# Optimization experiments

Measured on AMD Instinct MI355X. Metric: run time of the kernel, lower is better.

## Reference

```python
import jax, jax.numpy as jnp
import numpy as np

N_QUBITS = 4
N_LAYERS = 6
NUM_CLASSES = 10


def _apply_1q(state, gate, wire):
    # state: (B,2,2,2,2); gate: (2,2) shared or (B,2,2) per-sample
    s = jnp.moveaxis(state, wire + 1, -1)
    if gate.ndim == 3:
        s = jnp.einsum('bij,b...j->b...i', gate, s)
    else:
        s = jnp.einsum('ij,b...j->b...i', gate, s)
    return jnp.moveaxis(s, -1, wire + 1)


def _apply_cnot(state, c, t):
    s = jnp.moveaxis(state, (c + 1, t + 1), (-2, -1))
    s = jnp.stack([s[..., 0, :], s[..., 1, ::-1]], axis=-2)
    return jnp.moveaxis(s, (-2, -1), (c + 1, t + 1))


def _rot(phi, theta, omega):
    # PennyLane Rot = RZ(omega) @ RY(theta) @ RZ(phi)
    c, s = jnp.cos(theta / 2), jnp.sin(theta / 2)
    ep = jnp.exp(-0.5j * (phi + omega))
    em = jnp.exp(-0.5j * (phi - omega))
    return jnp.stack([
        jnp.stack([ep * c, -jnp.conj(em) * s]),
        jnp.stack([em * s, jnp.conj(ep) * c]),
    ])


def _quantum_net(angles, q_weights):
    # batched default.qubit statevector simulation, 4 wires
    B = angles.shape[0]
    state = jnp.zeros((B, 2, 2, 2, 2), jnp.complex64).at[:, 0, 0, 0, 0].set(1.0)
    # AngleEmbedding, rotation='Y' (per-sample RY gates)
    for w in range(N_QUBITS):
        a = angles[:, w]
        c, s = jnp.cos(a / 2), jnp.sin(a / 2)
        g = jnp.stack([jnp.stack([c, -s], -1), jnp.stack([s, c], -1)], -2)
        state = _apply_1q(state, g.astype(jnp.complex64), w)
    # StronglyEntanglingLayers: Rot on each wire, then ring of CNOTs with range r
    for l in range(N_LAYERS):
        for w in range(N_QUBITS):
            state = _apply_1q(state, _rot(q_weights[l, w, 0], q_weights[l, w, 1], q_weights[l, w, 2]), w)
        r = l % (N_QUBITS - 1) + 1
        for w in range(N_QUBITS):
            state = _apply_cnot(state, w, (w + r) % N_QUBITS)
    probs = jnp.abs(state) ** 2  # (B,2,2,2,2)
    z = jnp.array([1.0, -1.0], dtype=probs.dtype)
    exps = [jnp.einsum('bijkl,' + 'ijkl'[w] + '->b', probs, z) for w in range(N_QUBITS)]
    return jnp.stack(exps, -1)  # (B,4) expval PauliZ per wire


def setup_inputs() -> dict:
    key = jax.random.key(0)
    ks = jax.random.split(key, 6)
    B = 65536
    x = jax.random.normal(ks[0], (B, 512), jnp.float32)
    W_pre = jax.random.normal(ks[1], (N_QUBITS, 512), jnp.float32) / np.sqrt(512)
    b_pre = jax.random.normal(ks[2], (N_QUBITS,), jnp.float32) * 0.01
    q_weights = 0.01 * jax.random.normal(ks[3], (N_LAYERS, N_QUBITS, 3), jnp.float32)
    W_post = jax.random.normal(ks[4], (NUM_CLASSES, N_QUBITS), jnp.float32) / np.sqrt(N_QUBITS)
    b_post = jax.random.normal(ks[5], (NUM_CLASSES,), jnp.float32) * 0.01
    return {'x': x, 'W_pre': W_pre, 'b_pre': b_pre, 'q_weights': q_weights,
            'W_post': W_post, 'b_post': b_post}


def reference(x, W_pre, b_pre, q_weights, W_post, b_post):
    pre = x @ W_pre.T + b_pre                 # (B,4)
    angles = jnp.tanh(pre) * np.float32(np.pi)
    q_out = _quantum_net(angles, q_weights)   # (B,4)
    return q_out @ W_post.T + b_post          # (B,10)
```

## Files before the change

### kernel.cpp

```cpp
#include <hip/hip_runtime.h>
#include <math.h>

#define BLOCK 256
#define WAVES_PER_BLOCK 4
#define ROWS_PER_WAVE 8
#define ROWS_PER_BLOCK 32
#define K 512
#define K4 128
#define NQ 4
#define NL 6
#define NC 10

__global__ __launch_bounds__(BLOCK, 4) void vqc_fused_kernel(
    const float* __restrict__ x,
    const float* __restrict__ W_pre,
    const float* __restrict__ b_pre,
    const float* __restrict__ q_weights,
    const float* __restrict__ W_post,
    const float* __restrict__ b_post,
    float* __restrict__ out)
{
    __shared__ float gates[NL * NQ][8];
    __shared__ float angles_s[ROWS_PER_BLOCK][NQ];
    __shared__ float Wpost_s[NC * NQ];
    __shared__ float bpost_s[NC];
    __shared__ float bpre_s[NQ];

    const int tid  = threadIdx.x;
    const int wave = tid >> 6;
    const int lane = tid & 63;

    if (tid < NL * NQ) {
        const int l = tid >> 2, w = tid & 3;
        const float phi = q_weights[l * 12 + w * 3 + 0];
        const float th  = q_weights[l * 12 + w * 3 + 1];
        const float om  = q_weights[l * 12 + w * 3 + 2];
        const float c  = cosf(0.5f * th), s = sinf(0.5f * th);
        const float hp = 0.5f * (phi + om), hm = 0.5f * (phi - om);
        const float epr = cosf(hp), epi = -sinf(hp);
        const float emr = cosf(hm), emi = -sinf(hm);
        gates[tid][0] =  epr * c;  gates[tid][1] =  epi * c;
        gates[tid][2] = -emr * s;  gates[tid][3] =  emi * s;
        gates[tid][4] =  emr * s;  gates[tid][5] =  emi * s;
        gates[tid][6] =  epr * c;  gates[tid][7] = -epi * c;
    }
    if (tid >= 64 && tid < 64 + NC * NQ) Wpost_s[tid - 64] = W_post[tid - 64];
    if (tid >= 104 && tid < 104 + NC)    bpost_s[tid - 104] = b_post[tid - 104];
    if (tid >= 114 && tid < 114 + NQ)    bpre_s[tid - 114]  = b_pre[tid - 114];
    __syncthreads();

    const float4* x4 = (const float4*)x;
    const float4* W4 = (const float4*)W_pre;
    const float4 w0a = W4[0 * K4 + lane], w0b = W4[0 * K4 + 64 + lane];
    const float4 w1a = W4[1 * K4 + lane], w1b = W4[1 * K4 + 64 + lane];
    const float4 w2a = W4[2 * K4 + lane], w2b = W4[2 * K4 + 64 + lane];
    const float4 w3a = W4[3 * K4 + lane], w3b = W4[3 * K4 + 64 + lane];

    const int rowBase = blockIdx.x * ROWS_PER_BLOCK + wave * ROWS_PER_WAVE;

    #pragma unroll 4
    for (int rr = 0; rr < ROWS_PER_WAVE; ++rr) {
        const int r = rowBase + rr;
        const float4* xrow = x4 + (size_t)r * K4;
        const float4 xa = xrow[lane];
        const float4 xb = xrow[64 + lane];
        float acc0 = xa.x * w0a.x + xa.y * w0a.y + xa.z * w0a.z + xa.w * w0a.w
                   + xb.x * w0b.x + xb.y * w0b.y + xb.z * w0b.z + xb.w * w0b.w;
        float acc1 = xa.x * w1a.x + xa.y * w1a.y + xa.z * w1a.z + xa.w * w1a.w
                   + xb.x * w1b.x + xb.y * w1b.y + xb.z * w1b.z + xb.w * w1b.w;
        float acc2 = xa.x * w2a.x + xa.y * w2a.y + xa.z * w2a.z + xa.w * w2a.w
                   + xb.x * w2b.x + xb.y * w2b.y + xb.z * w2b.z + xb.w * w2b.w;
        float acc3 = xa.x * w3a.x + xa.y * w3a.y + xa.z * w3a.z + xa.w * w3a.w
                   + xb.x * w3b.x + xb.y * w3b.y + xb.z * w3b.z + xb.w * w3b.w;
        #pragma unroll
        for (int m = 1; m < 64; m <<= 1) {
            acc0 += __shfl_xor(acc0, m);
            acc1 += __shfl_xor(acc1, m);
            acc2 += __shfl_xor(acc2, m);
            acc3 += __shfl_xor(acc3, m);
        }
        if (lane < NQ) {
            const float accj = (lane == 0) ? acc0 : (lane == 1) ? acc1
                             : (lane == 2) ? acc2 : acc3;
            angles_s[wave * ROWS_PER_WAVE + rr][lane] =
                tanhf(accj + bpre_s[lane]) * 3.14159265358979323846f;
        }
    }
    __syncthreads();

    if (tid < ROWS_PER_BLOCK) {
        const int rl = tid;
        const int r  = blockIdx.x * ROWS_PER_BLOCK + rl;
        const float a0 = angles_s[rl][0], a1 = angles_s[rl][1];
        const float a2 = angles_s[rl][2], a3 = angles_s[rl][3];
        float c0, s0, c1, s1, c2, s2, c3, s3;
        __sincosf(0.5f * a0, &s0, &c0);
        __sincosf(0.5f * a1, &s1, &c1);
        __sincosf(0.5f * a2, &s2, &c2);
        __sincosf(0.5f * a3, &s3, &c3);

        float ar[16], ai[16];
        #pragma unroll
        for (int i = 0; i < 16; ++i) {
            ar[i] = ((i & 8) ? s0 : c0) * ((i & 4) ? s1 : c1)
                  * ((i & 2) ? s2 : c2) * ((i & 1) ? s3 : c3);
            ai[i] = 0.f;
        }

        #pragma unroll
        for (int l = 0; l < NL; ++l) {
            #pragma unroll
            for (int w = 0; w < NQ; ++w) {
                const float* G = gates[l * 4 + w];
                const float g00r = G[0], g00i = G[1], g01r = G[2], g01i = G[3];
                const float g10r = G[4], g10i = G[5], g11r = G[6], g11i = G[7];
                const int m = 8 >> w;
                #pragma unroll
                for (int i0 = 0; i0 < 16; ++i0) {
                    if (i0 & m) continue;
                    const int i1 = i0 | m;
                    const float A0r = ar[i0], A0i = ai[i0];
                    const float A1r = ar[i1], A1i = ai[i1];
                    ar[i0] = g00r * A0r - g00i * A0i + g01r * A1r - g01i * A1i;
                    ai[i0] = g00r * A0i + g00i * A0r + g01r * A1i + g01i * A1r;
                    ar[i1] = g10r * A0r - g10i * A0i + g11r * A1r - g11i * A1i;
                    ai[i1] = g10r * A0i + g10i * A0r + g11r * A1i + g11i * A1r;
                }
            }
            const int rshift = l % 3 + 1;
            #pragma unroll
            for (int w = 0; w < NQ; ++w) {
                const int cm = 8 >> w;
                const int tm = 8 >> ((w + rshift) & 3);
                #pragma unroll
                for (int i = 0; i < 16; ++i) {
                    if ((i & cm) && !(i & tm)) {
                        const int ii = i | tm;
                        float t;
                        t = ar[i]; ar[i] = ar[ii]; ar[ii] = t;
                        t = ai[i]; ai[i] = ai[ii]; ai[ii] = t;
                    }
                }
            }
        }

        float e0 = 0.f, e1 = 0.f, e2 = 0.f, e3 = 0.f;
        #pragma unroll
        for (int i = 0; i < 16; ++i) {
            const float p = ar[i] * ar[i] + ai[i] * ai[i];
            e0 += (i & 8) ? -p : p;
            e1 += (i & 4) ? -p : p;
            e2 += (i & 2) ? -p : p;
            e3 += (i & 1) ? -p : p;
        }

        float* orow = out + (size_t)r * NC;
        #pragma unroll
        for (int c = 0; c < NC; ++c) {
            orow[c] = bpost_s[c]
                    + Wpost_s[c * 4 + 0] * e0 + Wpost_s[c * 4 + 1] * e1
                    + Wpost_s[c * 4 + 2] * e2 + Wpost_s[c * 4 + 3] * e3;
        }
    }
}

extern "C" void kernel_launch(void* const* d_in, const int* in_sizes, int n_in,
                              void* d_out, int out_size, void* d_ws, size_t ws_size,
                              hipStream_t stream) {
    const float* x         = (const float*)d_in[0];
    const float* W_pre     = (const float*)d_in[1];
    const float* b_pre     = (const float*)d_in[2];
    const float* q_weights = (const float*)d_in[3];
    const float* W_post    = (const float*)d_in[4];
    const float* b_post    = (const float*)d_in[5];
    float* out = (float*)d_out;

    const int B = in_sizes[0] / K;
    dim3 grid(B / ROWS_PER_BLOCK);
    vqc_fused_kernel<<<grid, BLOCK, 0, stream>>>(x, W_pre, b_pre, q_weights,
                                                 W_post, b_post, out);
}
```

Measured before the change: 214.9 us.

## Split prenet GEMV and quantum simulation into separate kernels with full thread use

Splits the fused kernel in two. The first kernel computes the pre-net projection, prefetching the next row and using a transposed shuffle reduction that needs fewer shuffles, then writes the angles to workspace. The second kernel simulates the quantum circuit with one thread per row, so all 256 threads do work instead of only 32 per block sitting idle behind a barrier. The split adds a second launch and a small round trip through global memory; the first kernel also swaps tanhf for an exp-based approximation and the second writes its output with float2 stores.

```diff
diff --git a/kernel.cpp b/kernel.cpp
--- a/kernel.cpp
+++ b/kernel.cpp
@@ -1,34 +1,98 @@
 #include <hip/hip_runtime.h>
 #include <math.h>
 
-#define BLOCK 256
-#define WAVES_PER_BLOCK 4
-#define ROWS_PER_WAVE 8
-#define ROWS_PER_BLOCK 32
 #define K 512
 #define K4 128
 #define NQ 4
 #define NL 6
 #define NC 10
 
-__global__ __launch_bounds__(BLOCK, 4) void vqc_fused_kernel(
+#define A_BLOCK 256
+#define A_ROWS_PER_WAVE 8
+#define A_ROWS_PER_BLOCK 32
+
+__global__ __launch_bounds__(A_BLOCK, 4) void prenet_kernel(
     const float* __restrict__ x,
     const float* __restrict__ W_pre,
     const float* __restrict__ b_pre,
+    float* __restrict__ angles)
+{
+    const int tid  = threadIdx.x;
+    const int wave = tid >> 6;
+    const int lane = tid & 63;
+
+    const float4* x4 = (const float4*)x;
+    const float4* W4 = (const float4*)W_pre;
+    const float4 w0a = W4[0 * K4 + lane], w0b = W4[0 * K4 + 64 + lane];
+    const float4 w1a = W4[1 * K4 + lane], w1b = W4[1 * K4 + 64 + lane];
+    const float4 w2a = W4[2 * K4 + lane], w2b = W4[2 * K4 + 64 + lane];
+    const float4 w3a = W4[3 * K4 + lane], w3b = W4[3 * K4 + 64 + lane];
+    const float bp = (lane < NQ) ? b_pre[lane] : 0.f;
+
+    const int rowBase = blockIdx.x * A_ROWS_PER_BLOCK + wave * A_ROWS_PER_WAVE;
+    const float4* xrow0 = x4 + (size_t)rowBase * K4;
+    float4 xa = xrow0[lane];
+    float4 xb = xrow0[64 + lane];
+
+    #pragma unroll
+    for (int rr = 0; rr < A_ROWS_PER_WAVE; ++rr) {
+        float4 na = xa, nb = xb;
+        if (rr + 1 < A_ROWS_PER_WAVE) {
+            const float4* nx = x4 + (size_t)(rowBase + rr + 1) * K4;
+            na = nx[lane];
+            nb = nx[64 + lane];
+        }
+
+        float acc0 = xa.x * w0a.x + xa.y * w0a.y + xa.z * w0a.z + xa.w * w0a.w
+                   + xb.x * w0b.x + xb.y * w0b.y + xb.z * w0b.z + xb.w * w0b.w;
+        float acc1 = xa.x * w1a.x + xa.y * w1a.y + xa.z * w1a.z + xa.w * w1a.w
+                   + xb.x * w1b.x + xb.y * w1b.y + xb.z * w1b.z + xb.w * w1b.w;
+        float acc2 = xa.x * w2a.x + xa.y * w2a.y + xa.z * w2a.z + xa.w * w2a.w
+                   + xb.x * w2b.x + xb.y * w2b.y + xb.z * w2b.z + xb.w * w2b.w;
+        float acc3 = xa.x * w3a.x + xa.y * w3a.y + xa.z * w3a.z + xa.w * w3a.w
+                   + xb.x * w3b.x + xb.y * w3b.y + xb.z * w3b.z + xb.w * w3b.w;
+
+        const bool b0 = (lane & 1);
+        float pA = b0 ? acc1 : acc0;
+        float qA = b0 ? acc0 : acc1;
+        pA += __shfl_xor(qA, 1);
+        float pB = b0 ? acc3 : acc2;
+        float qB = b0 ? acc2 : acc3;
+        pB += __shfl_xor(qB, 1);
+        const bool b1 = (lane & 2);
+        float p = b1 ? pB : pA;
+        float q = b1 ? pA : pB;
+        p += __shfl_xor(q, 2);
+        p += __shfl_xor(p, 4);
+        p += __shfl_xor(p, 8);
+        p += __shfl_xor(p, 16);
+        p += __shfl_xor(p, 32);
+
+        if (lane < NQ) {
+            const float z = p + bp;
+            const float e = __expf(2.f * z);
+            const float th = 1.f - 2.f / (e + 1.f);
+            angles[(size_t)(rowBase + rr) * NQ + lane] =
+                th * 3.14159265358979323846f;
+        }
+        xa = na; xb = nb;
+    }
+}
+
+#define B_BLOCK 256
+
+__global__ __launch_bounds__(B_BLOCK, 4) void vqc_kernel(
+    const float* __restrict__ angles,
     const float* __restrict__ q_weights,
     const float* __restrict__ W_post,
     const float* __restrict__ b_post,
     float* __restrict__ out)
 {
     __shared__ float gates[NL * NQ][8];
-    __shared__ float angles_s[ROWS_PER_BLOCK][NQ];
     __shared__ float Wpost_s[NC * NQ];
     __shared__ float bpost_s[NC];
-    __shared__ float bpre_s[NQ];
-
-    const int tid  = threadIdx.x;
-    const int wave = tid >> 6;
-    const int lane = tid & 63;
+
+    const int tid = threadIdx.x;
 
     if (tid < NL * NQ) {
         const int l = tid >> 2, w = tid & 3;
@@ -46,122 +110,83 @@
     }
     if (tid >= 64 && tid < 64 + NC * NQ) Wpost_s[tid - 64] = W_post[tid - 64];
     if (tid >= 104 && tid < 104 + NC)    bpost_s[tid - 104] = b_post[tid - 104];
-    if (tid >= 114 && tid < 114 + NQ)    bpre_s[tid - 114]  = b_pre[tid - 114];
     __syncthreads();
 
-    const float4* x4 = (const float4*)x;
-    const float4* W4 = (const float4*)W_pre;
-    const float4 w0a = W4[0 * K4 + lane], w0b = W4[0 * K4 + 64 + lane];
-    const float4 w1a = W4[1 * K4 + lane], w1b = W4[1 * K4 + 64 + lane];
-    const float4 w2a = W4[2 * K4 + lane], w2b = W4[2 * K4 + 64 + lane];
-    const float4 w3a = W4[3 * K4 + lane], w3b = W4[3 * K4 + 64 + lane];
-
-    const int rowBase = blockIdx.x * ROWS_PER_BLOCK + wave * ROWS_PER_WAVE;
-
-    #pragma unroll 4
-    for (int rr = 0; rr < ROWS_PER_WAVE; ++rr) {
-        const int r = rowBase + rr;
-        const float4* xrow = x4 + (size_t)r * K4;
-        const float4 xa = xrow[lane];
-        const float4 xb = xrow[64 + lane];
-        float acc0 = xa.x * w0a.x + xa.y * w0a.y + xa.z * w0a.z + xa.w * w0a.w
-                   + xb.x * w0b.x + xb.y * w0b.y + xb.z * w0b.z + xb.w * w0b.w;
-        float acc1 = xa.x * w1a.x + xa.y * w1a.y + xa.z * w1a.z + xa.w * w1a.w
-                   + xb.x * w1b.x + xb.y * w1b.y + xb.z * w1b.z + xb.w * w1b.w;
-        float acc2 = xa.x * w2a.x + xa.y * w2a.y + xa.z * w2a.z + xa.w * w2a.w
-                   + xb.x * w2b.x + xb.y * w2b.y + xb.z * w2b.z + xb.w * w2b.w;
-        float acc3 = xa.x * w3a.x + xa.y * w3a.y + xa.z * w3a.z + xa.w * w3a.w
-                   + xb.x * w3b.x + xb.y * w3b.y + xb.z * w3b.z + xb.w * w3b.w;
+    const int r = blockIdx.x * B_BLOCK + tid;
+    const float4 a = ((const float4*)angles)[r];
+
+    float c0, s0, c1, s1, c2, s2, c3, s3;
+    __sincosf(0.5f * a.x, &s0, &c0);
+    __sincosf(0.5f * a.y, &s1, &c1);
+    __sincosf(0.5f * a.z, &s2, &c2);
+    __sincosf(0.5f * a.w, &s3, &c3);
+
+    float ar[16], ai[16];
+    #pragma unroll
+    for (int i = 0; i < 16; ++i) {
+        ar[i] = ((i & 8) ? s0 : c0) * ((i & 4) ? s1 : c1)
+              * ((i & 2) ? s2 : c2) * ((i & 1) ? s3 : c3);
+        ai[i] = 0.f;
+    }
+
+    #pragma unroll
+    for (int l = 0; l < NL; ++l) {
         #pragma unroll
-        for (int m = 1; m < 64; m <<= 1) {
-            acc0 += __shfl_xor(acc0, m);
-            acc1 += __shfl_xor(acc1, m);
-            acc2 += __shfl_xor(acc2, m);
-            acc3 += __shfl_xor(acc3, m);
-        }
-        if (lane < NQ) {
-            const float accj = (lane == 0) ? acc0 : (lane == 1) ? acc1
-                             : (lane == 2) ? acc2 : acc3;
-            angles_s[wave * ROWS_PER_WAVE + rr][lane] =
-                tanhf(accj + bpre_s[lane]) * 3.14159265358979323846f;
-        }
-    }
-    __syncthreads();
-
-    if (tid < ROWS_PER_BLOCK) {
-        const int rl = tid;
-        const int r  = blockIdx.x * ROWS_PER_BLOCK + rl;
-        const float a0 = angles_s[rl][0], a1 = angles_s[rl][1];
-        const float a2 = angles_s[rl][2], a3 = angles_s[rl][3];
-        float c0, s0, c1, s1, c2, s2, c3, s3;
-        __sincosf(0.5f * a0, &s0, &c0);
-        __sincosf(0.5f * a1, &s1, &c1);
-        __sincosf(0.5f * a2, &s2, &c2);
-        __sincosf(0.5f * a3, &s3, &c3);
-
-        float ar[16], ai[16];
+        for (int w = 0; w < NQ; ++w) {
+            const float* G = gates[l * 4 + w];
+            const float g00r = G[0], g00i = G[1], g01r = G[2], g01i = G[3];
+            const float g10r = G[4], g10i = G[5], g11r = G[6], g11i = G[7];
+            const int m = 8 >> w;
+            #pragma unroll
+            for (int i0 = 0; i0 < 16; ++i0) {
+                if (i0 & m) continue;
+                const int i1 = i0 | m;
+                const float A0r = ar[i0], A0i = ai[i0];
+                const float A1r = ar[i1], A1i = ai[i1];
+                ar[i0] = g00r * A0r - g00i * A0i + g01r * A1r - g01i * A1i;
+                ai[i0] = g00r * A0i + g00i * A0r + g01r * A1i + g01i * A1r;
+                ar[i1] = g10r * A0r - g10i * A0i + g11r * A1r - g11i * A1i;
+                ai[i1] = g10r * A0i + g10i * A0r + g11r * A1i + g11i * A1r;
+            }
+        }
+        const int rshift = l % 3 + 1;
         #pragma unroll
-        for (int i = 0; i < 16; ++i) {
-            ar[i] = ((i & 8) ? s0 : c0) * ((i & 4) ? s1 : c1)
-                  * ((i & 2) ? s2 : c2) * ((i & 1) ? s3 : c3);
-            ai[i] = 0.f;
-        }
-
-        #pragma unroll
-        for (int l = 0; l < NL; ++l) {
+        for (int w = 0; w < NQ; ++w) {
+            const int cm = 8 >> w;
+            const int tm = 8 >> ((w + rshift) & 3);
             #pragma unroll
-            for (int w = 0; w < NQ; ++w) {
-                const float* G = gates[l * 4 + w];
-                const float g00r = G[0], g00i = G[1], g01r = G[2], g01i = G[3];
-                const float g10r = G[4], g10i = G[5], g11r = G[6], g11i = G[7];
-                const int m = 8 >> w;
-                #pragma unroll
-                for (int i0 = 0; i0 < 16; ++i0) {
-                    if (i0 & m) continue;
-                    const int i1 = i0 | m;
-                    const float A0r = ar[i0], A0i = ai[i0];
-                    const float A1r = ar[i1], A1i = ai[i1];
-                    ar[i0] = g00r * A0r - g00i * A0i + g01r * A1r - g01i * A1i;
-                    ai[i0] = g00r * A0i + g00i * A0r + g01r * A1i + g01i * A1r;
-                    ar[i1] = g10r * A0r - g10i * A0i + g11r * A1r - g11i * A1i;
-                    ai[i1] = g10r * A0i + g10i * A0r + g11r * A1i + g11i * A1r;
+            for (int i = 0; i < 16; ++i) {
+                if ((i & cm) && !(i & tm)) {
+                    const int ii = i | tm;
+                    float t;
+                    t = ar[i]; ar[i] = ar[ii]; ar[ii] = t;
+                    t = ai[i]; ai[i] = ai[ii]; ai[ii] = t;
                 }
             }
-            const int rshift = l % 3 + 1;
-            #pragma unroll
-            for (int w = 0; w < NQ; ++w) {
-                const int cm = 8 >> w;
-                const int tm = 8 >> ((w + rshift) & 3);
-                #pragma unroll
-                for (int i = 0; i < 16; ++i) {
-                    if ((i & cm) && !(i & tm)) {
-                        const int ii = i | tm;
-                        float t;
-                        t = ar[i]; ar[i] = ar[ii]; ar[ii] = t;
-                        t = ai[i]; ai[i] = ai[ii]; ai[ii] = t;
-                    }
-                }
-            }
-        }
-
-        float e0 = 0.f, e1 = 0.f, e2 = 0.f, e3 = 0.f;
-        #pragma unroll
-        for (int i = 0; i < 16; ++i) {
-            const float p = ar[i] * ar[i] + ai[i] * ai[i];
-            e0 += (i & 8) ? -p : p;
-            e1 += (i & 4) ? -p : p;
-            e2 += (i & 2) ? -p : p;
-            e3 += (i & 1) ? -p : p;
-        }
-
-        float* orow = out + (size_t)r * NC;
-        #pragma unroll
-        for (int c = 0; c < NC; ++c) {
-            orow[c] = bpost_s[c]
-                    + Wpost_s[c * 4 + 0] * e0 + Wpost_s[c * 4 + 1] * e1
-                    + Wpost_s[c * 4 + 2] * e2 + Wpost_s[c * 4 + 3] * e3;
-        }
-    }
+        }
+    }
+
+    float e0 = 0.f, e1 = 0.f, e2 = 0.f, e3 = 0.f;
+    #pragma unroll
+    for (int i = 0; i < 16; ++i) {
+        const float pr = ar[i] * ar[i] + ai[i] * ai[i];
+        e0 += (i & 8) ? -pr : pr;
+        e1 += (i & 4) ? -pr : pr;
+        e2 += (i & 2) ? -pr : pr;
+        e3 += (i & 1) ? -pr : pr;
+    }
+
+    float o[NC];
+    #pragma unroll
+    for (int c = 0; c < NC; ++c) {
+        o[c] = bpost_s[c]
+             + Wpost_s[c * 4 + 0] * e0 + Wpost_s[c * 4 + 1] * e1
+             + Wpost_s[c * 4 + 2] * e2 + Wpost_s[c * 4 + 3] * e3;
+    }
+    float2* orow2 = (float2*)(out + (size_t)r * NC);
+    #pragma unroll
+    for (int c = 0; c < 5; ++c)
+        orow2[c] = make_float2(o[2 * c], o[2 * c + 1]);
 }
 
 extern "C" void kernel_launch(void* const* d_in, const int* in_sizes, int n_in,
@@ -173,10 +198,12 @@
     const float* q_weights = (const float*)d_in[3];
     const float* W_post    = (const float*)d_in[4];
     const float* b_post    = (const float*)d_in[5];
-    float* out = (float*)d_out;
+    float* out    = (float*)d_out;
+    float* angles = (float*)d_ws;
 
     const int B = in_sizes[0] / K;
-    dim3 grid(B / ROWS_PER_BLOCK);
-    vqc_fused_kernel<<<grid, BLOCK, 0, stream>>>(x, W_pre, b_pre, q_weights,
-                                                 W_post, b_post, out);
+    dim3 gridA(B / A_ROWS_PER_BLOCK);
+    prenet_kernel<<<gridA, A_BLOCK, 0, stream>>>(x, W_pre, b_pre, angles);
+    dim3 gridB(B / B_BLOCK);
+    vqc_kernel<<<gridB, B_BLOCK, 0, stream>>>(angles, q_weights, W_post, b_post, out);
 }
```

Measured after the change: 211.0 us. About the same (-1.8%).
